# Performance work log

Measured on AMD Instinct MI355X. Metric: run time of the kernel, lower is better.

Reference implementation:

```python
import jax, jax.numpy as jnp
import numpy as np

N = 400_000          # nodes
K = 50               # num_neighbors (incl. self); K-1 neighbors per node
E = N * (K - 1)      # edges = 19.6M
H = 128              # hidden size in NodeModel MLP
L = 2                # len(node_sizes) - 1 layers, node_sizes = [2,2,2]
D = 2                # node feature dim
MSG = D + 3          # msg_size = node_in + edge_size(3)


def setup_inputs() -> dict:
    key = jax.random.key(0)
    k1, k2, k3, k4, k5 = jax.random.split(key, 5)

    random_start = jax.random.normal(k1, (N, D), dtype=jnp.float32)

    # dst = repeat(range(N), K-1); src = kNN indices (random stand-in)
    dst = jnp.repeat(jnp.arange(N, dtype=jnp.int64), K - 1)
    src = jax.random.randint(k2, (E,), 0, N, dtype=jnp.int64)
    edge_index = jnp.stack([dst, src], axis=0)

    # edge_attr = [normalized true distance (1), direction (2)]
    dists = jax.random.uniform(k3, (E, 1), dtype=jnp.float32)
    dists = dists / jnp.max(dists)
    direction = random_start[dst] - random_start[src]
    edge_attr = jnp.concatenate([dists, direction], axis=1)  # [E, 3]

    # Per-layer MLP params: Linear(D+MSG, H) + ReLU, then Linear(H, D)
    ks = jax.random.split(k4, 2 * L)
    W1 = jnp.stack([jax.random.normal(ks[i], (D + MSG, H), dtype=jnp.float32)
                    * (1.0 / np.sqrt(D + MSG)) for i in range(L)])
    W2 = jnp.stack([jax.random.normal(ks[L + i], (H, D), dtype=jnp.float32)
                    * (1.0 / np.sqrt(H)) for i in range(L)])
    b1 = jnp.zeros((L, H), dtype=jnp.float32)
    b2 = jnp.zeros((L, D), dtype=jnp.float32)

    return {"random_start": random_start, "edge_index": edge_index,
            "edge_attr": edge_attr, "W1": W1, "b1": b1, "W2": W2, "b2": b2}


def reference(random_start, edge_index, edge_attr, W1, b1, W2, b2):
    x = random_start
    n = x.shape[0]
    dst, src = edge_index[0], edge_index[1]
    ones = jnp.ones((src.shape[0], 1), dtype=x.dtype)
    counts = jax.ops.segment_sum(ones, src, num_segments=n)  # [N,1]
    denom = jnp.maximum(counts, 1.0)

    for l in range(W1.shape[0]):
        # message: gather src node features + edge attrs
        msg = jnp.concatenate([x[src], edge_attr], axis=1)        # [E, D+3]
        agg = jax.ops.segment_sum(msg, src, num_segments=n) / denom  # scatter_mean by src (as in source)
        h = jnp.concatenate([x, agg], axis=1)                     # [N, 2D+3]
        h = jax.nn.relu(h @ W1[l] + b1[l])
        x = h @ W2[l] + b2[l]

    # fused per-edge squared euclidean distances (replaces the Python loop)
    diff = x[dst] - x[src]                                        # [E, D]
    proj_dists = jnp.sum(diff * diff, axis=1, keepdims=True)      # [E, 1]
    return proj_dists
```

## Files before the change

kernel.cpp:

```cpp
#include <hip/hip_runtime.h>


#define NB   196
#define BSH  11
#define BN   2048
#define TILE 2048
#define G1V  768
#define CAPV 208

typedef int   vint4   __attribute__((ext_vector_type(4)));
typedef float vfloat4 __attribute__((ext_vector_type(4)));

__device__ __forceinline__ unsigned long long make_rec(int id, float d, float v0, float v1) {
    unsigned int dq = __float2uint_rn(d * 4096.0f);
    unsigned int u0 = __float2uint_rn((v0 + 16.0f) * 256.0f);
    unsigned int u1 = __float2uint_rn((v1 + 16.0f) * 256.0f);
    return ((unsigned long long)(unsigned)id << 53) | ((unsigned long long)dq << 40)
         | ((unsigned long long)u0 << 20) | (unsigned long long)u1;
}

__global__ __launch_bounds__(256) void partition_kernel(
        const int* __restrict__ src,
        const float* __restrict__ attr,
        unsigned long long* __restrict__ records,
        unsigned int* __restrict__ counts,
        long long E, int G1, int cap, long long per) {
    __shared__ unsigned int pcur[NB];
    __shared__ unsigned int hist[NB];
    __shared__ unsigned int basev[NB];
    __shared__ unsigned long long resid[NB][8];
    __shared__ unsigned long long sortbuf[TILE];

    int t = threadIdx.x;
    for (int i = t; i < NB; i += 256) pcur[i] = 0;
    __syncthreads();

    int blk = blockIdx.x;
    long long bstart = (long long)blk * per;
    long long bend = bstart + per; if (bend > E) bend = E;

    for (long long tbeg = bstart; tbeg < bend; tbeg += TILE) {
        long long tend = tbeg + TILE; if (tend > bend) tend = bend;

        for (int i = t; i < NB; i += 256) hist[i] = 0;
        __syncthreads();

        unsigned long long rec[8]; int bkk[8]; unsigned offv[8];
        int m = 0;
        #pragma unroll
        for (int g = 0; g < 2; ++g) {
            long long e0 = tbeg + g * 1024 + 4 * t;
            if (e0 + 4 <= tend) {
                const vint4*   s4 = (const vint4*)(src + e0);
                const vfloat4* a4 = (const vfloat4*)(attr + e0 * 3);
                vint4 s    = __builtin_nontemporal_load(s4);
                vfloat4 a  = __builtin_nontemporal_load(a4);
                vfloat4 bb = __builtin_nontemporal_load(a4 + 1);
                vfloat4 c  = __builtin_nontemporal_load(a4 + 2);
                bkk[m] = s.x >> BSH; rec[m] = make_rec(s.x & (BN-1), a.x, a.y, a.z); m++;
                bkk[m] = s.y >> BSH; rec[m] = make_rec(s.y & (BN-1), a.w, bb.x, bb.y); m++;
                bkk[m] = s.z >> BSH; rec[m] = make_rec(s.z & (BN-1), bb.z, bb.w, c.x); m++;
                bkk[m] = s.w >> BSH; rec[m] = make_rec(s.w & (BN-1), c.y, c.z, c.w); m++;
            } else {
                for (long long e = e0; e < tend; ++e) {
                    int sv = src[e];
                    bkk[m] = sv >> BSH;
                    rec[m] = make_rec(sv & (BN-1), attr[e*3], attr[e*3+1], attr[e*3+2]);
                    m++;
                }
            }
        }

        for (int j = 0; j < m; ++j) offv[j] = atomicAdd(&hist[bkk[j]], 1u);
        __syncthreads();

        if (t < 64) {
            unsigned carry = 0;
            #pragma unroll
            for (int c = 0; c < (NB + 63) / 64; ++c) {
                int i = c * 64 + t;
                unsigned h = (i < NB) ? hist[i] : 0u;
                unsigned v = h;
                #pragma unroll
                for (int d = 1; d < 64; d <<= 1) {
                    unsigned u = __shfl_up(v, d, 64);
                    if (t >= d) v += u;
                }
                if (i < NB) basev[i] = carry + v - h;
                carry += __shfl(v, 63, 64);
            }
        }
        __syncthreads();

        for (int j = 0; j < m; ++j) sortbuf[basev[bkk[j]] + offv[j]] = rec[j];
        __syncthreads();

        if (t < NB) {
            int b = t;
            unsigned cnt = hist[b];
            unsigned p = pcur[b];
            unsigned r = p & 7u;
            unsigned flushed = p - r;
            unsigned total = r + cnt;
            unsigned nch = total >> 3;
            size_t gb = ((size_t)b * G1 + blk) * cap;
            unsigned sb = basev[b];
            for (unsigned ci = 0; ci < nch; ++ci) {
                unsigned gpos = flushed + ci * 8u;
                if (gpos + 8u <= (unsigned)cap) {
                    unsigned long long rc[8];
                    #pragma unroll
                    for (int k = 0; k < 8; ++k) {
                        unsigned idx = ci * 8u + (unsigned)k;
                        rc[k] = (idx < r) ? resid[b][idx] : sortbuf[sb + idx - r];
                    }
                    ulonglong2* dstp = (ulonglong2*)(records + gb + gpos);
                    dstp[0] = make_ulonglong2(rc[0], rc[1]);
                    dstp[1] = make_ulonglong2(rc[2], rc[3]);
                    dstp[2] = make_ulonglong2(rc[4], rc[5]);
                    dstp[3] = make_ulonglong2(rc[6], rc[7]);
                }
            }
            unsigned newr = total & 7u;
            unsigned long long tmp[8];
            for (unsigned k = 0; k < newr; ++k) {
                unsigned idx = nch * 8u + k;
                tmp[k] = (idx < r) ? resid[b][idx] : sortbuf[sb + idx - r];
            }
            for (unsigned k = 0; k < newr; ++k) resid[b][k] = tmp[k];
            pcur[b] = p + cnt;
        }
        __syncthreads();
    }

    if (t < NB) {
        int b = t;
        unsigned p = pcur[b];
        unsigned r = p & 7u;
        unsigned flushed = p - r;
        size_t gb = ((size_t)b * G1 + blk) * cap;
        for (unsigned k = 0; k < r; ++k) {
            unsigned gpos = flushed + k;
            if (gpos < (unsigned)cap) records[gb + gpos] = resid[b][k];
        }
        counts[(size_t)b * G1 + blk] = p < (unsigned)cap ? p : (unsigned)cap;
    }
}

__global__ __launch_bounds__(1024) void bucket_reduce(
        const unsigned long long* __restrict__ records,
        const unsigned int* __restrict__ counts,
        unsigned long long* __restrict__ part,
        int G1, int cap, int nsplit) {
    __shared__ unsigned long long acc[BN];
    for (int t = threadIdx.x; t < BN; t += 1024) acc[t] = 0ULL;
    __syncthreads();

    int b = blockIdx.x / nsplit;
    int s = blockIdx.x % nsplit;
    int regs = G1 / nsplit;
    int wave = threadIdx.x >> 6, lane = threadIdx.x & 63;

    for (int blk = s * regs + wave; blk < (s + 1) * regs; blk += 16) {
        unsigned c = counts[(size_t)b * G1 + blk];
        const unsigned long long* base = records + ((size_t)b * G1 + blk) * cap;
        for (unsigned r = lane; r < c; r += 64) {
            unsigned long long rec = __builtin_nontemporal_load(base + r);
            unsigned id  = (unsigned)(rec >> 53);
            unsigned long long dq  = (rec >> 40) & 0x1FFFULL;
            unsigned long long v0q = (rec >> 20) & 0x1FFFULL;
            unsigned long long v1q = rec & 0x1FFFULL;
            atomicAdd(&acc[id], (1ULL << 58) | (dq << 38) | (v0q << 19) | v1q);
        }
    }
    __syncthreads();
    unsigned long long* dstp = part + (size_t)s * (NB * BN) + (size_t)b * BN;
    for (int t = threadIdx.x; t < BN; t += 1024) dstp[t] = acc[t];
}

__global__ __launch_bounds__(256) void combine_mlp(
        const float* __restrict__ x_in,
        const unsigned long long* __restrict__ part,
        const float* __restrict__ W1, const float* __restrict__ b1,
        const float* __restrict__ W2, const float* __restrict__ b2,
        float* __restrict__ x_out, int N, int L, int nsplit) {
    __shared__ float W1s[2 * 7 * 128];
    __shared__ float b1s[2 * 128];
    __shared__ float W2s[2 * 128 * 2];
    __shared__ float b2s[2 * 2];
    for (int t = threadIdx.x; t < L * 7 * 128; t += 256) W1s[t] = W1[t];
    for (int t = threadIdx.x; t < L * 128; t += 256)     b1s[t] = b1[t];
    for (int t = threadIdx.x; t < L * 128 * 2; t += 256) W2s[t] = W2[t];
    for (int t = threadIdx.x; t < L * 2; t += 256)       b2s[t] = b2[t];
    __syncthreads();

    int i = blockIdx.x * 256 + threadIdx.x;
    if (i >= N) return;

    float2 xv = ((const float2*)x_in)[i];
    float x0 = xv.x, x1 = xv.y;

    int cnt = 0, sd = 0, s0 = 0, s1 = 0;
    for (int s = 0; s < nsplit; ++s) {
        unsigned long long v = part[(size_t)s * (NB * BN) + i];
        cnt += (int)(v >> 58);
        sd  += (int)((v >> 38) & 0xFFFFFULL);
        s0  += (int)((v >> 19) & 0x7FFFFULL);
        s1  += (int)(v & 0x7FFFFULL);
    }
    s0 -= cnt << 12;
    s1 -= cnt << 12;

    float denom = fmaxf((float)cnt, 1.0f);
    float mask  = (cnt > 0) ? 1.0f : 0.0f;
    float a0 = (float)sd * (1.0f / 4096.0f) / denom;
    float a1 = (float)s0 * (1.0f / 256.0f) / denom;
    float a2 = (float)s1 * (1.0f / 256.0f) / denom;

    for (int l = 0; l < L; ++l) {
        float m0 = mask * x0, m1 = mask * x1;
        const float* w1 = &W1s[l * 896];
        const float* w2 = &W2s[l * 256];
        const float* bb = &b1s[l * 128];
        float o0 = b2s[l * 2 + 0];
        float o1 = b2s[l * 2 + 1];
        #pragma unroll 8
        for (int j = 0; j < 128; ++j) {
            float h = bb[j];
            h = fmaf(x0, w1[0 * 128 + j], h);
            h = fmaf(x1, w1[1 * 128 + j], h);
            h = fmaf(m0, w1[2 * 128 + j], h);
            h = fmaf(m1, w1[3 * 128 + j], h);
            h = fmaf(a0, w1[4 * 128 + j], h);
            h = fmaf(a1, w1[5 * 128 + j], h);
            h = fmaf(a2, w1[6 * 128 + j], h);
            h = fmaxf(h, 0.0f);
            o0 = fmaf(h, w2[j * 2 + 0], o0);
            o1 = fmaf(h, w2[j * 2 + 1], o1);
        }
        x0 = o0; x1 = o1;
    }
    ((float2*)x_out)[i] = make_float2(x0, x1);
}

__device__ __forceinline__ unsigned long long pack_edge_fb(float d, float v0, float v1) {
    unsigned int ud = __float2uint_rn(d * 128.0f);
    unsigned int u0 = __float2uint_rn((v0 + 16.0f) * 128.0f);
    unsigned int u1 = __float2uint_rn((v1 + 16.0f) * 128.0f);
    return (1ULL << 55) | ((unsigned long long)ud << 40)
         | ((unsigned long long)u0 << 20) | (unsigned long long)u1;
}

__global__ __launch_bounds__(256) void scatter_fb(
        const int* __restrict__ src, const float* __restrict__ attr,
        unsigned long long* __restrict__ acc, long long E) {
    long long E4 = E >> 2;
    long long stride = (long long)gridDim.x * blockDim.x;
    long long t0 = (long long)blockIdx.x * blockDim.x + threadIdx.x;
    const vint4* src4 = (const vint4*)src;
    const vfloat4* attr4 = (const vfloat4*)attr;
    for (long long t = t0; t < E4; t += stride) {
        vint4 s = src4[t];
        vfloat4 a = attr4[t*3+0]; vfloat4 b = attr4[t*3+1]; vfloat4 c = attr4[t*3+2];
        atomicAdd(&acc[s.x], pack_edge_fb(a.x, a.y, a.z));
        atomicAdd(&acc[s.y], pack_edge_fb(a.w, b.x, b.y));
        atomicAdd(&acc[s.z], pack_edge_fb(b.z, b.w, c.x));
        atomicAdd(&acc[s.w], pack_edge_fb(c.y, c.z, c.w));
    }
    for (long long e = E4*4 + t0; e < E; e += stride)
        atomicAdd(&acc[src[e]], pack_edge_fb(attr[e*3], attr[e*3+1], attr[e*3+2]));
}

__global__ __launch_bounds__(256) void mlp_fb(
        const float* __restrict__ x_in,
        const unsigned long long* __restrict__ acc,
        const float* __restrict__ W1, const float* __restrict__ b1,
        const float* __restrict__ W2, const float* __restrict__ b2,
        float* __restrict__ x_out, int N, int L) {
    __shared__ float W1s[2 * 7 * 128];
    __shared__ float b1s[2 * 128];
    __shared__ float W2s[2 * 128 * 2];
    __shared__ float b2s[2 * 2];
    for (int t = threadIdx.x; t < L * 7 * 128; t += 256) W1s[t] = W1[t];
    for (int t = threadIdx.x; t < L * 128; t += 256)     b1s[t] = b1[t];
    for (int t = threadIdx.x; t < L * 128 * 2; t += 256) W2s[t] = W2[t];
    for (int t = threadIdx.x; t < L * 2; t += 256)       b2s[t] = b2[t];
    __syncthreads();

    int i = blockIdx.x * 256 + threadIdx.x;
    if (i >= N) return;
    float2 xv = ((const float2*)x_in)[i];
    float x0 = xv.x, x1 = xv.y;

    unsigned long long e0 = acc[i];
    int cnti = (int)(e0 >> 55);
    int sumd = (int)((e0 >> 40) & 0x7FFF);
    int s0 = (int)((e0 >> 20) & 0xFFFFF) - (cnti << 11);
    int s1 = (int)(e0 & 0xFFFFF) - (cnti << 11);

    float denom = fmaxf((float)cnti, 1.0f);
    float mask  = (cnti > 0) ? 1.0f : 0.0f;
    float inv = (1.0f / 128.0f) / denom;
    float a0 = (float)sumd * inv;
    float a1 = (float)s0 * inv;
    float a2 = (float)s1 * inv;

    for (int l = 0; l < L; ++l) {
        float m0 = mask * x0, m1 = mask * x1;
        const float* w1 = &W1s[l * 896];
        const float* w2 = &W2s[l * 256];
        const float* bb = &b1s[l * 128];
        float o0 = b2s[l * 2 + 0];
        float o1 = b2s[l * 2 + 1];
        #pragma unroll 8
        for (int j = 0; j < 128; ++j) {
            float h = bb[j];
            h = fmaf(x0, w1[0 * 128 + j], h);
            h = fmaf(x1, w1[1 * 128 + j], h);
            h = fmaf(m0, w1[2 * 128 + j], h);
            h = fmaf(m1, w1[3 * 128 + j], h);
            h = fmaf(a0, w1[4 * 128 + j], h);
            h = fmaf(a1, w1[5 * 128 + j], h);
            h = fmaf(a2, w1[6 * 128 + j], h);
            h = fmaxf(h, 0.0f);
            o0 = fmaf(h, w2[j * 2 + 0], o0);
            o1 = fmaf(h, w2[j * 2 + 1], o1);
        }
        x0 = o0; x1 = o1;
    }
    ((float2*)x_out)[i] = make_float2(x0, x1);
}

__global__ __launch_bounds__(256) void edge_out_kernel(
        const int* __restrict__ dst,
        const int* __restrict__ src,
        const float2* __restrict__ x2,
        float* __restrict__ out,
        long long E, double invK, int derived) {
    long long stride = (long long)gridDim.x * blockDim.x;
    long long t0 = (long long)blockIdx.x * blockDim.x + threadIdx.x;
    long long E4 = E >> 2;
    const vint4* src4 = (const vint4*)src;
    const vint4* dst4 = (const vint4*)dst;
    for (long long t = t0; t < E4; t += stride) {
        long long e = t * 4;
        vint4 s = __builtin_nontemporal_load(src4 + t);
        int d0, d1, d2, d3;
        if (derived) {
            d0 = (int)(((double)e + 0.5) * invK);
            d1 = (int)(((double)e + 1.5) * invK);
            d2 = (int)(((double)e + 2.5) * invK);
            d3 = (int)(((double)e + 3.5) * invK);
        } else {
            vint4 d = __builtin_nontemporal_load(dst4 + t);
            d0 = d.x; d1 = d.y; d2 = d.z; d3 = d.w;
        }
        float2 xd0 = x2[d0], xs0 = x2[s.x];
        float2 xd1 = x2[d1], xs1 = x2[s.y];
        float2 xd2 = x2[d2], xs2 = x2[s.z];
        float2 xd3 = x2[d3], xs3 = x2[s.w];
        vfloat4 r; float ax, ay;
        ax = xd0.x - xs0.x; ay = xd0.y - xs0.y; r.x = ax*ax + ay*ay;
        ax = xd1.x - xs1.x; ay = xd1.y - xs1.y; r.y = ax*ax + ay*ay;
        ax = xd2.x - xs2.x; ay = xd2.y - xs2.y; r.z = ax*ax + ay*ay;
        ax = xd3.x - xs3.x; ay = xd3.y - xs3.y; r.w = ax*ax + ay*ay;
        __builtin_nontemporal_store(r, (vfloat4*)out + t);
    }
    for (long long e = E4*4 + t0; e < E; e += stride) {
        int dd = derived ? (int)(((double)e + 0.5) * invK) : dst[e];
        float2 xd = x2[dd], xs = x2[src[e]];
        float dx = xd.x - xs.x, dy = xd.y - xs.y;
        out[e] = dx*dx + dy*dy;
    }
}

extern "C" void kernel_launch(void* const* d_in, const int* in_sizes, int n_in,
                              void* d_out, int out_size, void* d_ws, size_t ws_size,
                              hipStream_t stream) {
    const float* random_start = (const float*)d_in[0];
    const int*   edge_index   = (const int*)d_in[1];
    const float* edge_attr    = (const float*)d_in[2];
    const float* W1 = (const float*)d_in[3];
    const float* b1 = (const float*)d_in[4];
    const float* W2 = (const float*)d_in[5];
    const float* b2 = (const float*)d_in[6];

    int       N = in_sizes[0] / 2;
    long long E = in_sizes[1] / 2;
    int       L = in_sizes[3] / (7 * 128);

    const int* dst = edge_index;
    const int* src = edge_index + E;

    int derived = (N > 0 && E % N == 0) ? 1 : 0;
    long long K1 = derived ? (E / N) : 1;
    double invK = derived ? (1.0 / (double)K1) : 1.0;

    const int TB = 256;
    int nblocks = (N + TB - 1) / TB;

    const int G1 = G1V, cap = CAPV;

    size_t x2_off      = 0;
    size_t counts_off  = x2_off + (size_t)N * 8;
    size_t records_off = counts_off + (size_t)NB * G1 * 4;
    records_off = (records_off + 15) & ~(size_t)15;
    size_t part_off    = records_off + (size_t)NB * G1 * cap * 8;
    part_off = (part_off + 15) & ~(size_t)15;

    float* x2 = (float*)((char*)d_ws + x2_off);

    int nsplit = 0;
    if (N <= NB * BN && ws_size > part_off) {
        size_t leftover = ws_size - part_off;
        nsplit = (int)(leftover / ((size_t)NB * BN * 8));
        if (nsplit > 4) nsplit = 4;
        if (nsplit == 3 && (G1 % 3) != 0) nsplit = 2;
    }

    if (nsplit >= 1) {
        unsigned int* counts = (unsigned int*)((char*)d_ws + counts_off);
        unsigned long long* records = (unsigned long long*)((char*)d_ws + records_off);
        unsigned long long* part = (unsigned long long*)((char*)d_ws + part_off);
        long long per = (((E + G1 - 1) / G1) + 7) & ~7LL;

        partition_kernel<<<G1, TB, 0, stream>>>(src, edge_attr, records, counts, E, G1, cap, per);
        bucket_reduce<<<NB * nsplit, 1024, 0, stream>>>(records, counts, part, G1, cap, nsplit);
        combine_mlp<<<nblocks, TB, 0, stream>>>(random_start, part, W1, b1, W2, b2,
                                                x2, N, L, nsplit);
    } else {
        unsigned long long* acc_old = (unsigned long long*)((char*)d_ws + counts_off);
        (void)hipMemsetAsync(acc_old, 0, (size_t)N * 8, stream);
        scatter_fb<<<8192, TB, 0, stream>>>(src, edge_attr, acc_old, E);
        mlp_fb<<<nblocks, TB, 0, stream>>>(random_start, acc_old, W1, b1, W2, b2, x2, N, L);
    }

    edge_out_kernel<<<8192, TB, 0, stream>>>(dst, src, (const float2*)x2,
                                             (float*)d_out, E, invK, derived);
}
```

Before: 350.0 us.

## Parallelize bucket chunk flush across threads and vectorize bucket record loads

The partition kernel now packs each bucket's histogram count and running position into one shared word, scans both record offsets and 8-record chunk offsets, and distributes chunk flushes across all 256 threads using a binary search. Previously one thread per bucket wrote that bucket's chunks serially, which left work unbalanced. The bucket reduce kernel loads two records per 128-bit nontemporal load and writes its partial sums with nontemporal stores. The packing limits per-bucket counts and offsets to 16 bits and adds a binary search per chunk.

```diff
diff --git a/kernel.cpp b/kernel.cpp
--- a/kernel.cpp
+++ b/kernel.cpp
@@ -10,6 +10,7 @@
 
 typedef int   vint4   __attribute__((ext_vector_type(4)));
 typedef float vfloat4 __attribute__((ext_vector_type(4)));
+typedef unsigned long long vu64x2 __attribute__((ext_vector_type(2)));
 
 __device__ __forceinline__ unsigned long long make_rec(int id, float d, float v0, float v1) {
     unsigned int dq = __float2uint_rn(d * 4096.0f);
@@ -25,14 +26,14 @@
         unsigned long long* __restrict__ records,
         unsigned int* __restrict__ counts,
         long long E, int G1, int cap, long long per) {
-    __shared__ unsigned int pcur[NB];
-    __shared__ unsigned int hist[NB];
-    __shared__ unsigned int basev[NB];
+    __shared__ unsigned int cnt_pc[NB];
+    __shared__ unsigned int scanpk[NB];
     __shared__ unsigned long long resid[NB][8];
     __shared__ unsigned long long sortbuf[TILE];
+    __shared__ unsigned int nchunks_s;
 
     int t = threadIdx.x;
-    for (int i = t; i < NB; i += 256) pcur[i] = 0;
+    for (int i = t; i < NB; i += 256) cnt_pc[i] = 0;
     __syncthreads();
 
     int blk = blockIdx.x;
@@ -41,9 +42,6 @@
 
     for (long long tbeg = bstart; tbeg < bend; tbeg += TILE) {
         long long tend = tbeg + TILE; if (tend > bend) tend = bend;
-
-        for (int i = t; i < NB; i += 256) hist[i] = 0;
-        __syncthreads();
 
         unsigned long long rec[8]; int bkk[8]; unsigned offv[8];
         int m = 0;
@@ -71,71 +69,94 @@
             }
         }
 
-        for (int j = 0; j < m; ++j) offv[j] = atomicAdd(&hist[bkk[j]], 1u);
+        for (int j = 0; j < m; ++j) offv[j] = atomicAdd(&cnt_pc[bkk[j]], 1u) & 0xFFFFu;
         __syncthreads();
 
         if (t < 64) {
-            unsigned carry = 0;
+            unsigned carryA = 0, carryB = 0;
             #pragma unroll
             for (int c = 0; c < (NB + 63) / 64; ++c) {
                 int i = c * 64 + t;
-                unsigned h = (i < NB) ? hist[i] : 0u;
+                unsigned cp = (i < NB) ? cnt_pc[i] : 0u;
+                unsigned h = cp & 0xFFFFu;
+                unsigned p = cp >> 16;
+                unsigned n = ((p & 7u) + h) >> 3;
                 unsigned v = h;
                 #pragma unroll
                 for (int d = 1; d < 64; d <<= 1) {
                     unsigned u = __shfl_up(v, d, 64);
                     if (t >= d) v += u;
                 }
-                if (i < NB) basev[i] = carry + v - h;
-                carry += __shfl(v, 63, 64);
+                unsigned w = n;
+                #pragma unroll
+                for (int d = 1; d < 64; d <<= 1) {
+                    unsigned u = __shfl_up(w, d, 64);
+                    if (t >= d) w += u;
+                }
+                if (i < NB)
+                    scanpk[i] = (carryA + v - h) | ((carryB + w - n) << 16);
+                carryA += __shfl(v, 63, 64);
+                carryB += __shfl(w, 63, 64);
             }
+            if (t == 0) nchunks_s = carryB;
         }
         __syncthreads();
 
-        for (int j = 0; j < m; ++j) sortbuf[basev[bkk[j]] + offv[j]] = rec[j];
+        for (int j = 0; j < m; ++j)
+            sortbuf[(scanpk[bkk[j]] & 0xFFFFu) + offv[j]] = rec[j];
+        __syncthreads();
+
+        unsigned nchunks = nchunks_s;
+        for (unsigned cid = t; cid < nchunks; cid += 256) {
+            int lo = 0, hi = NB - 1;
+            while (lo < hi) {
+                int mid = (lo + hi + 1) >> 1;
+                if ((scanpk[mid] >> 16) <= cid) lo = mid; else hi = mid - 1;
+            }
+            int b = lo;
+            unsigned ci = cid - (scanpk[b] >> 16);
+            unsigned p = cnt_pc[b] >> 16;
+            unsigned r = p & 7u;
+            unsigned gpos = (p - r) + ci * 8u;
+            if (gpos + 8u <= (unsigned)cap) {
+                unsigned sb = scanpk[b] & 0xFFFFu;
+                unsigned long long rc[8];
+                #pragma unroll
+                for (int k = 0; k < 8; ++k) {
+                    unsigned idx = ci * 8u + (unsigned)k;
+                    rc[k] = (idx < r) ? resid[b][idx] : sortbuf[sb + idx - r];
+                }
+                ulonglong2* dstp = (ulonglong2*)(records + ((size_t)b * G1 + blk) * cap + gpos);
+                dstp[0] = make_ulonglong2(rc[0], rc[1]);
+                dstp[1] = make_ulonglong2(rc[2], rc[3]);
+                dstp[2] = make_ulonglong2(rc[4], rc[5]);
+                dstp[3] = make_ulonglong2(rc[6], rc[7]);
+            }
+        }
         __syncthreads();
 
         if (t < NB) {
             int b = t;
-            unsigned cnt = hist[b];
-            unsigned p = pcur[b];
+            unsigned cp = cnt_pc[b];
+            unsigned cnt = cp & 0xFFFFu;
+            unsigned p = cp >> 16;
             unsigned r = p & 7u;
-            unsigned flushed = p - r;
             unsigned total = r + cnt;
             unsigned nch = total >> 3;
-            size_t gb = ((size_t)b * G1 + blk) * cap;
-            unsigned sb = basev[b];
-            for (unsigned ci = 0; ci < nch; ++ci) {
-                unsigned gpos = flushed + ci * 8u;
-                if (gpos + 8u <= (unsigned)cap) {
-                    unsigned long long rc[8];
-                    #pragma unroll
-                    for (int k = 0; k < 8; ++k) {
-                        unsigned idx = ci * 8u + (unsigned)k;
-                        rc[k] = (idx < r) ? resid[b][idx] : sortbuf[sb + idx - r];
-                    }
-                    ulonglong2* dstp = (ulonglong2*)(records + gb + gpos);
-                    dstp[0] = make_ulonglong2(rc[0], rc[1]);
-                    dstp[1] = make_ulonglong2(rc[2], rc[3]);
-                    dstp[2] = make_ulonglong2(rc[4], rc[5]);
-                    dstp[3] = make_ulonglong2(rc[6], rc[7]);
-                }
-            }
             unsigned newr = total & 7u;
-            unsigned long long tmp[8];
+            unsigned sb = scanpk[b] & 0xFFFFu;
             for (unsigned k = 0; k < newr; ++k) {
                 unsigned idx = nch * 8u + k;
-                tmp[k] = (idx < r) ? resid[b][idx] : sortbuf[sb + idx - r];
+                resid[b][k] = (idx < r) ? resid[b][idx] : sortbuf[sb + idx - r];
             }
-            for (unsigned k = 0; k < newr; ++k) resid[b][k] = tmp[k];
-            pcur[b] = p + cnt;
+            cnt_pc[b] = (p + cnt) << 16;
         }
         __syncthreads();
     }
 
     if (t < NB) {
         int b = t;
-        unsigned p = pcur[b];
+        unsigned p = cnt_pc[b] >> 16;
         unsigned r = p & 7u;
         unsigned flushed = p - r;
         size_t gb = ((size_t)b * G1 + blk) * cap;
@@ -164,18 +185,29 @@
     for (int blk = s * regs + wave; blk < (s + 1) * regs; blk += 16) {
         unsigned c = counts[(size_t)b * G1 + blk];
         const unsigned long long* base = records + ((size_t)b * G1 + blk) * cap;
-        for (unsigned r = lane; r < c; r += 64) {
-            unsigned long long rec = __builtin_nontemporal_load(base + r);
-            unsigned id  = (unsigned)(rec >> 53);
-            unsigned long long dq  = (rec >> 40) & 0x1FFFULL;
-            unsigned long long v0q = (rec >> 20) & 0x1FFFULL;
-            unsigned long long v1q = rec & 0x1FFFULL;
-            atomicAdd(&acc[id], (1ULL << 58) | (dq << 38) | (v0q << 19) | v1q);
+        const vu64x2* base2 = (const vu64x2*)base;
+        unsigned c2 = c >> 1;
+        for (unsigned r = lane; r < c2; r += 64) {
+            vu64x2 rr = __builtin_nontemporal_load(base2 + r);
+            unsigned long long r0 = rr.x, r1 = rr.y;
+            unsigned id0 = (unsigned)(r0 >> 53);
+            atomicAdd(&acc[id0], (1ULL << 58) | (((r0 >> 40) & 0x1FFFULL) << 38)
+                               | (((r0 >> 20) & 0x1FFFULL) << 19) | (r0 & 0x1FFFULL));
+            unsigned id1 = (unsigned)(r1 >> 53);
+            atomicAdd(&acc[id1], (1ULL << 58) | (((r1 >> 40) & 0x1FFFULL) << 38)
+                               | (((r1 >> 20) & 0x1FFFULL) << 19) | (r1 & 0x1FFFULL));
+        }
+        if (lane == 0 && (c & 1u)) {
+            unsigned long long r0 = base[c - 1];
+            unsigned id0 = (unsigned)(r0 >> 53);
+            atomicAdd(&acc[id0], (1ULL << 58) | (((r0 >> 40) & 0x1FFFULL) << 38)
+                               | (((r0 >> 20) & 0x1FFFULL) << 19) | (r0 & 0x1FFFULL));
         }
     }
     __syncthreads();
     unsigned long long* dstp = part + (size_t)s * (NB * BN) + (size_t)b * BN;
-    for (int t = threadIdx.x; t < BN; t += 1024) dstp[t] = acc[t];
+    for (int t = threadIdx.x; t < BN; t += 1024)
+        __builtin_nontemporal_store(acc[t], dstp + t);
 }
 
 __global__ __launch_bounds__(256) void combine_mlp(
```

After: 345.7 us. No clear change (-1.2%).
